# Optimization experiments

Hardware: AMD Instinct MI355X
Metric: run time of the kernel (lower is better)

Reference implementation:

```python
import jax, jax.numpy as jnp
import numpy as np

THRESHOLD = 0.5
NEG_POS_RATIO = 3
ALPHA = 1.0


def cxcy_to_xy(c):
    return jnp.concatenate([c[..., :2] - c[..., 2:] / 2, c[..., :2] + c[..., 2:] / 2], axis=-1)


def xy_to_cxcy(x):
    return jnp.concatenate([(x[..., :2] + x[..., 2:]) / 2, x[..., 2:] - x[..., :2]], axis=-1)


def cxcy_to_gcxgcy(cxcy, priors_cxcy):
    return jnp.concatenate([
        (cxcy[..., :2] - priors_cxcy[..., :2]) / (priors_cxcy[..., 2:] / 10.0),
        jnp.log(cxcy[..., 2:] / priors_cxcy[..., 2:]) * 5.0,
    ], axis=-1)


def jaccard(a, b):
    # a: [M,4] xy, b: [P,4] xy -> IoU [M,P]
    lt = jnp.maximum(a[:, None, :2], b[None, :, :2])
    rb = jnp.minimum(a[:, None, 2:], b[None, :, 2:])
    wh = jnp.clip(rb - lt, 0.0)
    inter = wh[..., 0] * wh[..., 1]
    area_a = (a[:, 2] - a[:, 0]) * (a[:, 3] - a[:, 1])
    area_b = (b[:, 2] - b[:, 0]) * (b[:, 3] - b[:, 1])
    return inter / (area_a[:, None] + area_b[None, :] - inter)


def setup_inputs() -> dict:
    key = jax.random.key(0)
    k1, k2, k3, k4, k5, k6, k7 = jax.random.split(key, 7)
    B, P, C, M = 32, 8732, 81, 20
    predicted_locs = jax.random.normal(k1, (B, P, 4), dtype=jnp.float32)
    predicted_scores = jax.random.normal(k2, (B, P, C), dtype=jnp.float32)
    # priors in cxcy format, well inside the unit square
    p_cxy = jax.random.uniform(k3, (P, 2), minval=0.05, maxval=0.95)
    p_wh = jax.random.uniform(k4, (P, 2), minval=0.05, maxval=0.30)
    priors_cxcy = jnp.concatenate([p_cxy, p_wh], axis=-1).astype(jnp.float32)
    # GT boxes: random cxcy -> xy, clipped to [0,1]
    b_cxy = jax.random.uniform(k5, (B, M, 2), minval=0.1, maxval=0.9)
    b_wh = jax.random.uniform(k6, (B, M, 2), minval=0.05, maxval=0.40)
    boxes = jnp.clip(cxcy_to_xy(jnp.concatenate([b_cxy, b_wh], axis=-1)), 0.0, 1.0).astype(jnp.float32)
    labels = jax.random.randint(k7, (B, M), 1, C, dtype=jnp.int64 if jax.config.jax_enable_x64 else jnp.int32)
    return {
        "predicted_locs": predicted_locs,
        "predicted_scores": predicted_scores,
        "boxes": boxes,
        "labels": labels,
        "priors_cxcy": priors_cxcy,
    }


def _match_one(boxes_i, labels_i, priors_cxcy, priors_xy):
    M = boxes_i.shape[0]
    overlap = jaccard(boxes_i, priors_xy)                 # [M, P]
    ov_per_prior = overlap.max(axis=0)                    # [P]
    obj_per_prior = overlap.argmax(axis=0)                # [P]
    prior_per_obj = overlap.argmax(axis=1)                # [M]
    # force-assign each object to its best prior
    obj_per_prior = obj_per_prior.at[prior_per_obj].set(jnp.arange(M))
    ov_per_prior = ov_per_prior.at[prior_per_obj].set(1.0)
    lab = labels_i[obj_per_prior]                         # [P]
    lab = jnp.where(ov_per_prior < THRESHOLD, 0, lab)
    true_locs = cxcy_to_gcxgcy(xy_to_cxcy(boxes_i[obj_per_prior]), priors_cxcy)  # [P,4]
    return true_locs, lab


def reference(predicted_locs, predicted_scores, boxes, labels, priors_cxcy):
    priors_xy = cxcy_to_xy(priors_cxcy)
    true_locs, true_classes = jax.vmap(_match_one, in_axes=(0, 0, None, None))(
        boxes, labels, priors_cxcy, priors_xy)            # [B,P,4], [B,P]

    pos = true_classes > 0                                # [B,P]
    n_pos = pos.sum(axis=1)                               # [B]
    n_pos_total = n_pos.sum().astype(jnp.float32)

    # smooth L1 over positive priors (mean over all selected elements)
    d = predicted_locs - true_locs
    ad = jnp.abs(d)
    sl1 = jnp.where(ad < 1.0, 0.5 * d * d, ad - 0.5)      # [B,P,4]
    loc_loss = jnp.sum(sl1 * pos[..., None]) / (n_pos_total * 4.0)

    # per-prior cross entropy
    logp = jax.nn.log_softmax(predicted_scores, axis=-1)
    ce = -jnp.take_along_axis(logp, true_classes[..., None], axis=-1)[..., 0]  # [B,P]

    conf_pos = jnp.sum(jnp.where(pos, ce, 0.0))
    neg = jnp.where(pos, 0.0, ce)
    neg_sorted = -jnp.sort(-neg, axis=1)                  # descending per image
    ranks = jnp.arange(neg.shape[1])[None, :]
    hard = ranks < (NEG_POS_RATIO * n_pos)[:, None]
    conf_neg = jnp.sum(neg_sorted * hard)

    conf_loss = (conf_neg + conf_pos) / n_pos_total
    return conf_loss, ALPHA * loc_loss
```

## Files before the change

kernel.cpp:

```cpp
#include <hip/hip_runtime.h>
#include <math.h>

#define NB 32
#define NP 8732
#define NC 81
#define NM 20
#define CHUNKS 35
#define NROWS (NB * NP)
#define NGROUPS (NROWS / 4)
#define LSE_BLOCKS ((NGROUPS + 63) / 64)
#define MATCH_BLOCKS (NB * CHUNKS)
#define EPI_BLOCKS ((NROWS + 255) / 256)
#define MT 1024
#define MV 9

typedef unsigned long long ull;
#define AGENT __HIP_MEMORY_SCOPE_AGENT


__global__ __launch_bounds__(256)
void lse_match_kernel(const float* __restrict__ scores,
                      float* __restrict__ lse,
                      const float* __restrict__ boxes,
                      const int*   __restrict__ labels,
                      const float* __restrict__ priors,
                      ull*      __restrict__ bestpart,
                      unsigned* __restrict__ labobj,
                      int*      __restrict__ chunkdone)
{
    __shared__ float bxs[NM][4];
    __shared__ float areaA[NM];
    __shared__ int   labL[NM];
    __shared__ float iouT[256 * 21];
    __shared__ ull   wcand[4][NM];
    __shared__ int   flagLast;
    __shared__ int   pps[NM];

    const int tid = threadIdx.x;

    if (blockIdx.x < LSE_BLOCKS) {
        const int q = tid & 3;
        const long long g = (long long)blockIdx.x * 64 + (tid >> 2);
        const bool gvalid = g < NGROUPS;
        const float4* gp = reinterpret_cast<const float4*>(scores) + (gvalid ? g : 0) * 81;

        float s0 = 0.f, s1 = 0.f, s2 = 0.f, s3 = 0.f;
#pragma unroll
        for (int j = 0; j < 20; j++) {
            const float4 A = gp[q + 4 * j];
            float ex = __expf(A.x), ey = __expf(A.y), ez = __expf(A.z), ew = __expf(A.w);
            if (j <= 4) {
                s0 += (ex + ey) + (ez + ew);
            } else if (j >= 6 && j <= 9) {
                s1 += (ex + ey) + (ez + ew);
            } else if (j >= 11 && j <= 14) {
                s2 += (ex + ey) + (ez + ew);
            } else if (j >= 16) {
                s3 += (ex + ey) + (ez + ew);
            } else {
                const int bnd = (j == 5) ? 81 : (j == 10) ? 162 : 243;
                const int e0 = (q + 4 * j) * 4;
                float lo_ = ((e0     < bnd) ? ex : 0.f) + ((e0 + 1 < bnd) ? ey : 0.f)
                          + ((e0 + 2 < bnd) ? ez : 0.f) + ((e0 + 3 < bnd) ? ew : 0.f);
                float hi_ = ((e0     < bnd) ? 0.f : ex) + ((e0 + 1 < bnd) ? 0.f : ey)
                          + ((e0 + 2 < bnd) ? 0.f : ez) + ((e0 + 3 < bnd) ? 0.f : ew);
                if (j == 5)      { s0 += lo_; s1 += hi_; }
                else if (j == 10){ s1 += lo_; s2 += hi_; }
                else             { s2 += lo_; s3 += hi_; }
            }
        }
        if (q == 0) {
            const float4 L = gp[80];
            s3 += (__expf(L.x) + __expf(L.y)) + (__expf(L.z) + __expf(L.w));
        }
        s0 += __shfl_xor(s0, 1);  s0 += __shfl_xor(s0, 2);
        s1 += __shfl_xor(s1, 1);  s1 += __shfl_xor(s1, 2);
        s2 += __shfl_xor(s2, 1);  s2 += __shfl_xor(s2, 2);
        s3 += __shfl_xor(s3, 1);  s3 += __shfl_xor(s3, 2);

        if (gvalid) {
            const float srow = (q == 0) ? s0 : (q == 1) ? s1 : (q == 2) ? s2 : s3;
            lse[g * 4 + q] = __logf(srow);
        }
        return;
    }

    const int mbid = blockIdx.x - LSE_BLOCKS;
    const int b = mbid / CHUNKS;
    const int chunk = mbid % CHUNKS;
    const int p = chunk * 256 + tid;
    const bool valid = p < NP;

    if (tid < NM * 4) ((float*)bxs)[tid] = boxes[b * NM * 4 + tid];
    if (tid >= 128 && tid < 128 + NM) labL[tid - 128] = labels[b * NM + (tid - 128)];
    if (tid == 0) flagLast = 0;
    __syncthreads();
    if (tid < NM) areaA[tid] = (bxs[tid][2] - bxs[tid][0]) * (bxs[tid][3] - bxs[tid][1]);
    __syncthreads();

    float4 pc = reinterpret_cast<const float4*>(priors)[valid ? p : 0];
    const float px1 = pc.x - pc.z * 0.5f;
    const float py1 = pc.y - pc.w * 0.5f;
    const float px2 = pc.x + pc.z * 0.5f;
    const float py2 = pc.y + pc.w * 0.5f;
    const float pa  = (px2 - px1) * (py2 - py1);

    float bov = -1.f; int bm = 0;
    const int tbase = tid * 21;
#pragma unroll
    for (int m = 0; m < NM; m++) {
        float ix1 = fmaxf(bxs[m][0], px1);
        float iy1 = fmaxf(bxs[m][1], py1);
        float ix2 = fminf(bxs[m][2], px2);
        float iy2 = fminf(bxs[m][3], py2);
        float iw = fmaxf(ix2 - ix1, 0.f);
        float ih = fmaxf(iy2 - iy1, 0.f);
        float inter = iw * ih;
        float iou = inter / (areaA[m] + pa - inter);
        if (iou > bov) { bov = iou; bm = m; }
        iouT[tbase + m] = valid ? iou : -1.f;
    }
    if (valid) {
        int lab = (bov < 0.5f) ? 0 : labL[bm];
        __hip_atomic_store(&labobj[(size_t)b * NP + p],
                           (unsigned)lab | ((unsigned)bm << 8),
                           __ATOMIC_RELAXED, AGENT);
    }
    __syncthreads();

    const int lane = tid & 63, wid = tid >> 6;
    if (lane < NM) {
        const int m = lane;
        float bv = -1.f; int bt = 0;
        const int t0 = wid * 64;
        for (int t = t0; t < t0 + 64; t++) {
            float v = iouT[t * 21 + m];
            if (v > bv) { bv = v; bt = t; }
        }
        wcand[wid][m] = (bv < 0.f) ? 0ull
            : ((((ull)__float_as_uint(bv)) << 32) | (unsigned)~(unsigned)(chunk * 256 + bt));
    }
    __syncthreads();
    if (tid < NM) {
        ull k = wcand[0][tid];
        if (wcand[1][tid] > k) k = wcand[1][tid];
        if (wcand[2][tid] > k) k = wcand[2][tid];
        if (wcand[3][tid] > k) k = wcand[3][tid];
        __hip_atomic_store(&bestpart[(size_t)(b * CHUNKS + chunk) * NM + tid], k,
                           __ATOMIC_RELAXED, AGENT);
    }
    __syncthreads();
    if (tid == 0) {
        int old = __hip_atomic_fetch_add(&chunkdone[b], 1, __ATOMIC_ACQ_REL, AGENT);
        if (old == CHUNKS - 1) flagLast = 1;
    }
    __syncthreads();

    if (flagLast) {
        if (tid < NM) {
            ull k = 0ull;
            for (int c = 0; c < CHUNKS; c++) {
                ull v = __hip_atomic_load(&bestpart[(size_t)(b * CHUNKS + c) * NM + tid],
                                          __ATOMIC_RELAXED, AGENT);
                if (v > k) k = v;
            }
            pps[tid] = (int)~(unsigned)(k & 0xFFFFFFFFull);
        }
        __syncthreads();
        if (tid < NM) {
            int pp = pps[tid];
            bool win = true;
            for (int m2 = tid + 1; m2 < NM; m2++)
                if (pps[m2] == pp) win = false;
            if (win)
                __hip_atomic_store(&labobj[(size_t)b * NP + pp],
                                   (unsigned)labL[tid] | ((unsigned)tid << 8),
                                   __ATOMIC_RELAXED, AGENT);
        }
    }
}

__global__ __launch_bounds__(256)
void epilogue_kernel(const float* __restrict__ scores,
                     const float* __restrict__ plocs,
                     const float* __restrict__ boxes,
                     const float* __restrict__ priors,
                     const unsigned* __restrict__ labobj,
                     const float* __restrict__ lse,
                     float* __restrict__ neg,
                     float* __restrict__ perimgPos,
                     float* __restrict__ perimgLoc,
                     int*   __restrict__ nposarr)
{
    __shared__ float bsum, blocsum;
    __shared__ int   bnp[2];
    const int tid = threadIdx.x;
    if (tid == 0) { bsum = 0.f; blocsum = 0.f; }
    if (tid < 2) bnp[tid] = 0;
    __syncthreads();

    const int r = blockIdx.x * 256 + tid;
    const bool valid = r < NROWS;
    const int rr = valid ? r : 0;
    const int b = rr / NP;
    const int p = rr - b * NP;
    const int bfirst = (blockIdx.x * 256) / NP;

    const unsigned lo = labobj[rr];
    const int lab = lo & 0xFF;
    const int obj = lo >> 8;
    const float labval = scores[(size_t)rr * NC + lab];
    const float ce = lse[rr] - labval;

    if (valid) {
        if (lab > 0) {
            neg[r] = 0.f;
            atomicAdd(&bsum, ce);
            atomicAdd(&bnp[b - bfirst], 1);
            float4 pcr = reinterpret_cast<const float4*>(priors)[p];
            const float* bx = boxes + ((size_t)b * NM + obj) * 4;
            float x1 = bx[0], y1 = bx[1], x2 = bx[2], y2 = bx[3];
            float bcx = (x1 + x2) * 0.5f, bcy = (y1 + y2) * 0.5f;
            float bw = x2 - x1, bh = y2 - y1;
            float g0 = (bcx - pcr.x) / (pcr.z / 10.f);
            float g1 = (bcy - pcr.y) / (pcr.w / 10.f);
            float g2 = __logf(bw / pcr.z) * 5.f;
            float g3 = __logf(bh / pcr.w) * 5.f;
            float4 pl = reinterpret_cast<const float4*>(plocs)[rr];
            float t = 0.f, d, ad;
            d = pl.x - g0; ad = fabsf(d); t += (ad < 1.f) ? 0.5f * d * d : ad - 0.5f;
            d = pl.y - g1; ad = fabsf(d); t += (ad < 1.f) ? 0.5f * d * d : ad - 0.5f;
            d = pl.z - g2; ad = fabsf(d); t += (ad < 1.f) ? 0.5f * d * d : ad - 0.5f;
            d = pl.w - g3; ad = fabsf(d); t += (ad < 1.f) ? 0.5f * d * d : ad - 0.5f;
            atomicAdd(&blocsum, t);
        } else {
            neg[r] = ce;
        }
    }
    __syncthreads();
    if (tid == 0) {
        if (bsum != 0.f)    atomicAdd(&perimgPos[bfirst], bsum);
        if (blocsum != 0.f) atomicAdd(&perimgLoc[bfirst], blocsum);
        if (bnp[0] > 0)     atomicAdd(&nposarr[bfirst], bnp[0]);
        if (bnp[1] > 0 && bfirst + 1 < NB) atomicAdd(&nposarr[bfirst + 1], bnp[1]);
    }
}

__global__ __launch_bounds__(MT)
void mine_kernel(const float* __restrict__ neg,
                 const int*   __restrict__ nposarr,
                 const float* __restrict__ perimgPos,
                 const float* __restrict__ perimgLoc,
                 float* __restrict__ acc,
                 float* __restrict__ out)
{
    __shared__ int      hist[2048];
    __shared__ unsigned bres;
    __shared__ int      kkS;
    __shared__ unsigned tbits;
    __shared__ float    redF[MT / 64];
    __shared__ int      redI[MT / 64];

    const int b = blockIdx.x;
    const int tid = threadIdx.x;
    const int lane = tid & 63, wid = tid >> 6;

    float v[MV];
    unsigned mask = 0u;
    const float* src = neg + (size_t)b * NP;
#pragma unroll
    for (int j = 0; j < MV; j++) {
        const int idx = tid + MT * j;
        const bool ok = idx < NP;
        v[j] = ok ? src[idx] : -1.f;
        if (ok) mask |= (1u << j);
    }
    int k = nposarr[b] * 3;
    if (k > NP) k = NP;

    float t = 0.f;
    if (k > 0) {
        float lo = -0.5f;
        float R  = 16.5f;
        if (tid == 0) kkS = k;

        for (int pass = 0; pass < 2; pass++) {
            hist[tid] = 0;
            hist[tid + 1024] = 0;
            __syncthreads();
            const float invw = 2048.f / R;
#pragma unroll
            for (int j = 0; j < MV; j++) {
                if (mask & (1u << j)) {
                    int bin = (int)((v[j] - lo) * invw);
                    bin = (bin < 0) ? 0 : (bin > 2047 ? 2047 : bin);
                    atomicAdd(&hist[bin], 1);
                }
            }
            __syncthreads();
            if (wid == 0) {
                const int kkC = kkS;
                const int base = lane * 32;
                int sL = 0;
#pragma unroll
                for (int i = 0; i < 32; i++) sL += hist[base + i];
                int val = sL;
#pragma unroll
                for (int off = 1; off < 64; off <<= 1) {
                    int tmp = __shfl_down(val, off);
                    if (lane + off < 64) val += tmp;
                }
                const int sufAfter = val - sL;
                if (sufAfter < kkC && kkC <= sufAfter + sL) {
                    int cum = sufAfter;
                    int Bstar = base;
                    int cAbove = sufAfter;
                    for (int i = 31; i >= 0; i--) {
                        const int h = hist[base + i];
                        if (cum + h >= kkC) { Bstar = base + i; cAbove = cum; break; }
                        cum += h;
                    }
                    bres = (unsigned)Bstar;
                    kkS = kkC - cAbove;
                }
            }
            __syncthreads();
            const unsigned Bs = bres;
            const float w = R / 2048.f;
#pragma unroll
            for (int j = 0; j < MV; j++) {
                if (mask & (1u << j)) {
                    int bin = (int)((v[j] - lo) * invw);
                    bin = (bin < 0) ? 0 : (bin > 2047 ? 2047 : bin);
                    if (bin != (int)Bs) mask &= ~(1u << j);
                }
            }
            lo += (float)Bs * w;
            R = w;
        }
        if (tid == 0) tbits = 0u;
        __syncthreads();
        unsigned mb = 0u;
#pragma unroll
        for (int j = 0; j < MV; j++)
            if ((mask & (1u << j)) && v[j] >= 0.f) {
                const unsigned bitsj = __float_as_uint(v[j]);
                if (bitsj > mb) mb = bitsj;
            }
#pragma unroll
        for (int off = 32; off; off >>= 1) {
            const unsigned o = __shfl_xor(mb, off);
            if (o > mb) mb = o;
        }
        if (lane == 0) atomicMax(&tbits, mb);
        __syncthreads();
        t = __uint_as_float(tbits);
    }

    float s = 0.f; int cg = 0;
#pragma unroll
    for (int j = 0; j < MV; j++) {
        const float val = v[j];
        if (val > t) { s += val; cg++; }
    }
#pragma unroll
    for (int off = 32; off; off >>= 1) { s += __shfl_down(s, off); cg += __shfl_down(cg, off); }
    if (lane == 0) { redF[wid] = s; redI[wid] = cg; }
    __syncthreads();
    if (tid == 0) {
        float sum = 0.f; int cG = 0;
#pragma unroll
        for (int w = 0; w < MT / 64; w++) { sum += redF[w]; cG += redI[w]; }
        const float contrib = (k > 0) ? (sum + (float)(k - cG) * t) : 0.f;
        atomicAdd(&acc[2], contrib);
        atomicAdd(&acc[1], perimgPos[b]);
        atomicAdd(&acc[0], perimgLoc[b]);
        __threadfence();
        int old = atomicAdd((int*)acc + 3, 1);
        if (old == NB - 1) {
            __threadfence();
            float nt = 0.f;
            for (int i = 0; i < NB; i++) nt += (float)nposarr[i];
            out[0] = (acc[2] + acc[1]) / nt;
            out[1] = acc[0] / (nt * 4.f);
        }
    }
}

extern "C" void kernel_launch(void* const* d_in, const int* in_sizes, int n_in,
                              void* d_out, int out_size, void* d_ws, size_t ws_size,
                              hipStream_t stream)
{
    const float* plocs  = (const float*)d_in[0];
    const float* scores = (const float*)d_in[1];
    const float* boxes  = (const float*)d_in[2];
    const int*   labels = (const int*)d_in[3];
    const float* priors = (const float*)d_in[4];
    float* out = (float*)d_out;

    char* base = (char*)d_ws;
    float*    acc       = (float*)base;
    int*      nposarr   = (int*)(base + 64);
    int*      chunkdone = (int*)(base + 192);
    float*    perimgPos = (float*)(base + 320);
    float*    perimgLoc = (float*)(base + 448);
    ull*      bestpart  = (ull*)(base + 4096);
    unsigned* labobj    = (unsigned*)(base + 196608);
    float*    neg       = (float*)(base + 1314304);
    float*    lse       = (float*)(base + 2432000);

    hipMemsetAsync(d_ws, 0, 4096, stream);
    hipLaunchKernelGGL(lse_match_kernel, dim3(LSE_BLOCKS + MATCH_BLOCKS), dim3(256), 0, stream,
                       scores, lse, boxes, labels, priors, bestpart, labobj, chunkdone);
    hipLaunchKernelGGL(epilogue_kernel, dim3(EPI_BLOCKS), dim3(256), 0, stream,
                       scores, plocs, boxes, priors, labobj, lse, neg,
                       perimgPos, perimgLoc, nposarr);
    hipLaunchKernelGGL(mine_kernel, dim3(NB), dim3(MT), 0, stream,
                       neg, nposarr, perimgPos, perimgLoc, acc, out);
}
```

Baseline: 71.18 us.

## Restructure log-sum-exp to wave-per-16-rows coalesced loads with LDS atomics

The log-sum-exp pass now gives each wavefront 16 contiguous score rows. Lanes read consecutive float4s, so the loads are fully coalesced, and each lane adds its exp values into per-row shared-memory sums with LDS atomics instead of a strided 4-lanes-per-group layout. Match blocks are moved to the front of the grid so the dependent chunk work starts first. The cost is LDS atomic contention per row, and the wsums initialisation is read back without a barrier (it relies on wave-synchronous execution).

```diff
diff --git a/kernel.cpp b/kernel.cpp
--- a/kernel.cpp
+++ b/kernel.cpp
@@ -7,8 +7,8 @@
 #define NM 20
 #define CHUNKS 35
 #define NROWS (NB * NP)
-#define NGROUPS (NROWS / 4)
-#define LSE_BLOCKS ((NGROUPS + 63) / 64)
+#define NWAVES (NROWS / 16)
+#define LSE_BLOCKS (NWAVES / 4)
 #define MATCH_BLOCKS (NB * CHUNKS)
 #define EPI_BLOCKS ((NROWS + 255) / 256)
 #define MT 1024
@@ -35,57 +35,53 @@
     __shared__ ull   wcand[4][NM];
     __shared__ int   flagLast;
     __shared__ int   pps[NM];
+    __shared__ float wsums[4][16];
 
     const int tid = threadIdx.x;
-
-    if (blockIdx.x < LSE_BLOCKS) {
-        const int q = tid & 3;
-        const long long g = (long long)blockIdx.x * 64 + (tid >> 2);
-        const bool gvalid = g < NGROUPS;
-        const float4* gp = reinterpret_cast<const float4*>(scores) + (gvalid ? g : 0) * 81;
-
-        float s0 = 0.f, s1 = 0.f, s2 = 0.f, s3 = 0.f;
-#pragma unroll
-        for (int j = 0; j < 20; j++) {
-            const float4 A = gp[q + 4 * j];
-            float ex = __expf(A.x), ey = __expf(A.y), ez = __expf(A.z), ew = __expf(A.w);
-            if (j <= 4) {
-                s0 += (ex + ey) + (ez + ew);
-            } else if (j >= 6 && j <= 9) {
-                s1 += (ex + ey) + (ez + ew);
-            } else if (j >= 11 && j <= 14) {
-                s2 += (ex + ey) + (ez + ew);
-            } else if (j >= 16) {
-                s3 += (ex + ey) + (ez + ew);
-            } else {
-                const int bnd = (j == 5) ? 81 : (j == 10) ? 162 : 243;
-                const int e0 = (q + 4 * j) * 4;
-                float lo_ = ((e0     < bnd) ? ex : 0.f) + ((e0 + 1 < bnd) ? ey : 0.f)
-                          + ((e0 + 2 < bnd) ? ez : 0.f) + ((e0 + 3 < bnd) ? ew : 0.f);
-                float hi_ = ((e0     < bnd) ? 0.f : ex) + ((e0 + 1 < bnd) ? 0.f : ey)
-                          + ((e0 + 2 < bnd) ? 0.f : ez) + ((e0 + 3 < bnd) ? 0.f : ew);
-                if (j == 5)      { s0 += lo_; s1 += hi_; }
-                else if (j == 10){ s1 += lo_; s2 += hi_; }
-                else             { s2 += lo_; s3 += hi_; }
-            }
-        }
-        if (q == 0) {
-            const float4 L = gp[80];
-            s3 += (__expf(L.x) + __expf(L.y)) + (__expf(L.z) + __expf(L.w));
-        }
-        s0 += __shfl_xor(s0, 1);  s0 += __shfl_xor(s0, 2);
-        s1 += __shfl_xor(s1, 1);  s1 += __shfl_xor(s1, 2);
-        s2 += __shfl_xor(s2, 1);  s2 += __shfl_xor(s2, 2);
-        s3 += __shfl_xor(s3, 1);  s3 += __shfl_xor(s3, 2);
-
-        if (gvalid) {
-            const float srow = (q == 0) ? s0 : (q == 1) ? s1 : (q == 2) ? s2 : s3;
-            lse[g * 4 + q] = __logf(srow);
+    const int lane = tid & 63, w = tid >> 6;
+
+    if (blockIdx.x >= MATCH_BLOCKS) {
+        const int gwave = (blockIdx.x - MATCH_BLOCKS) * 4 + w;
+        const float4* base4 = reinterpret_cast<const float4*>(scores) + (size_t)gwave * 324;
+
+        if (lane < 16) wsums[w][lane] = 0.f;
+
+        float4 val0 = base4[lane];
+        float4 val1 = base4[64 + lane];
+        float4 val2 = base4[128 + lane];
+        float4 val3 = base4[192 + lane];
+        float4 val4 = base4[256 + lane];
+        float4 tail;
+        if (lane < 4) tail = base4[320 + lane];
+
+#pragma unroll
+        for (int k = 0; k < 5; k++) {
+            const float4 A = (k == 0) ? val0 : (k == 1) ? val1 : (k == 2) ? val2
+                           : (k == 3) ? val3 : val4;
+            const int e0 = (64 * k + lane) * 4;
+            const int rowA = e0 / 81;
+            const int r0 = e0 - rowA * 81;
+            const float ex = __expf(A.x), ey = __expf(A.y),
+                        ez = __expf(A.z), ew = __expf(A.w);
+            float lo_ = ex, hi_ = 0.f;
+            if (r0 < 80) lo_ += ey; else hi_ += ey;
+            if (r0 < 79) lo_ += ez; else hi_ += ez;
+            if (r0 < 78) lo_ += ew; else hi_ += ew;
+            atomicAdd(&wsums[w][rowA], lo_);
+            if (hi_ != 0.f) atomicAdd(&wsums[w][rowA + 1], hi_);
+        }
+        if (lane < 4) {
+            const float s = (__expf(tail.x) + __expf(tail.y))
+                          + (__expf(tail.z) + __expf(tail.w));
+            atomicAdd(&wsums[w][15], s);
+        }
+        if (lane < 16) {
+            lse[(size_t)gwave * 16 + lane] = __logf(wsums[w][lane]);
         }
         return;
     }
 
-    const int mbid = blockIdx.x - LSE_BLOCKS;
+    const int mbid = blockIdx.x;
     const int b = mbid / CHUNKS;
     const int chunk = mbid % CHUNKS;
     const int p = chunk * 256 + tid;
@@ -128,16 +124,15 @@
     }
     __syncthreads();
 
-    const int lane = tid & 63, wid = tid >> 6;
     if (lane < NM) {
         const int m = lane;
         float bv = -1.f; int bt = 0;
-        const int t0 = wid * 64;
+        const int t0 = w * 64;
         for (int t = t0; t < t0 + 64; t++) {
             float v = iouT[t * 21 + m];
             if (v > bv) { bv = v; bt = t; }
         }
-        wcand[wid][m] = (bv < 0.f) ? 0ull
+        wcand[w][m] = (bv < 0.f) ? 0ull
             : ((((ull)__float_as_uint(bv)) << 32) | (unsigned)~(unsigned)(chunk * 256 + bt));
     }
     __syncthreads();
@@ -410,7 +405,7 @@
     float*    lse       = (float*)(base + 2432000);
 
     hipMemsetAsync(d_ws, 0, 4096, stream);
-    hipLaunchKernelGGL(lse_match_kernel, dim3(LSE_BLOCKS + MATCH_BLOCKS), dim3(256), 0, stream,
+    hipLaunchKernelGGL(lse_match_kernel, dim3(MATCH_BLOCKS + LSE_BLOCKS), dim3(256), 0, stream,
                        scores, lse, boxes, labels, priors, bestpart, labobj, chunkdone);
     hipLaunchKernelGGL(epilogue_kernel, dim3(EPI_BLOCKS), dim3(256), 0, stream,
                        scores, plocs, boxes, priors, labobj, lse, neg,
```

Result: slower. 107.8 us (+51.4%).
